# Kernel tuning notes

Hardware: AMD Instinct MI355X
Metric: run time of the kernel (lower is better)

## Reference

```python
import jax, jax.numpy as jnp
import numpy as np

NUM_KEYS = 64

def setup_inputs() -> dict:
    key = jax.random.key(0)
    k1, k2 = jax.random.split(key)
    inputs = jax.random.randint(k1, (8, 4096, 1024), 0, NUM_KEYS, dtype=jnp.int32)
    # learned per-key bias (build() creates shape (num_keys,) for key_shape=[1])
    b = jax.random.normal(k2, (NUM_KEYS,), dtype=jnp.float32)
    # keys are sorted unique scalars (0..63), stored as float like the TF cast
    keys = jnp.arange(NUM_KEYS, dtype=jnp.float32)
    return {"inputs": inputs, "b": b, "keys": keys}


def reference(inputs, b, keys):
    # Original math: out = sum_k (inputs == keys[k]) * b[k], elementwise over inputs.
    # With unique sorted keys this is a gather: find the matching key index per
    # element and pick b there; elements matching no key contribute 0.
    # This avoids the O(num_keys * numel) broadcast blow-up of the TF graph.
    xf = inputs.astype(jnp.float32)
    K = keys.shape[0]
    idx = jnp.clip(jnp.searchsorted(keys, xf), 0, K - 1)  # [8,4096,1024]
    out = jnp.where(keys[idx] == xf, b[idx], jnp.float32(0.0))
    return out
```

## Files before the change

kernel.cpp:

```cpp
#include <hip/hip_runtime.h>

#define NKEYS 64
#define UNROLL 4

typedef int   __attribute__((ext_vector_type(4))) i32x4;
typedef float __attribute__((ext_vector_type(4))) f32x4;

__global__ __launch_bounds__(256) void sel_xform_kernel(
    const i32x4* __restrict__ in,
    const float* __restrict__ b,
    const float* __restrict__ keys,
    f32x4* __restrict__ out,
    int nvec, int ntail, const int* __restrict__ in_tail, float* __restrict__ out_tail)
{
    __shared__ float t[NKEYS];
    const int tid = threadIdx.x;
    if (tid < NKEYS) t[tid] = 0.0f;
    __syncthreads();
    if (tid < NKEYS) {
        const float kv = keys[tid];
        const int iv = (int)kv;
        if ((float)iv == kv && iv >= 0 && iv < NKEYS) {
            t[iv] = b[tid];
        }
    }
    __syncthreads();

    const int B = blockDim.x;
    const int chunk = gridDim.x * B * UNROLL;

    auto lut4 = [&](i32x4 v) -> f32x4 {
        const float rx = t[v.x & 63];
        const float ry = t[v.y & 63];
        const float rz = t[v.z & 63];
        const float rw = t[v.w & 63];
        f32x4 o;
        o.x = ((unsigned)v.x < NKEYS) ? rx : 0.0f;
        o.y = ((unsigned)v.y < NKEYS) ? ry : 0.0f;
        o.z = ((unsigned)v.z < NKEYS) ? rz : 0.0f;
        o.w = ((unsigned)v.w < NKEYS) ? rw : 0.0f;
        return o;
    };

    for (int base = blockIdx.x * B * UNROLL; base < nvec; base += chunk) {
        if (base + UNROLL * B <= nvec) {
            const int i0 = base + tid;
            const i32x4 v0 = __builtin_nontemporal_load(in + i0);
            const i32x4 v1 = __builtin_nontemporal_load(in + i0 + B);
            const i32x4 v2 = __builtin_nontemporal_load(in + i0 + 2 * B);
            const i32x4 v3 = __builtin_nontemporal_load(in + i0 + 3 * B);

            out[i0]         = lut4(v0);
            out[i0 + B]     = lut4(v1);
            out[i0 + 2 * B] = lut4(v2);
            out[i0 + 3 * B] = lut4(v3);
        } else {
            for (int j = 0; j < UNROLL; ++j) {
                const int i = base + j * B + tid;
                if (i < nvec) {
                    const i32x4 v = __builtin_nontemporal_load(in + i);
                    out[i] = lut4(v);
                }
            }
        }
    }

    if (blockIdx.x == 0 && tid < ntail) {
        const int v = in_tail[tid];
        out_tail[tid] = ((unsigned)v < NKEYS) ? t[v] : 0.0f;
    }
}

extern "C" void kernel_launch(void* const* d_in, const int* in_sizes, int n_in,
                              void* d_out, int out_size, void* d_ws, size_t ws_size,
                              hipStream_t stream) {
    const int*   x    = (const int*)d_in[0];
    const float* b    = (const float*)d_in[1];
    const float* keys = (const float*)d_in[2];
    float* out = (float*)d_out;

    const int n    = in_sizes[0];
    const int nvec = n >> 2;
    const int ntail = n & 3;

    const int block = 256;
    int grid = (nvec + block * UNROLL - 1) / (block * UNROLL);
    if (grid > 2048) grid = 2048;
    if (grid < 1) grid = 1;

    sel_xform_kernel<<<grid, block, 0, stream>>>(
        (const i32x4*)x, b, keys, (f32x4*)out,
        nvec, ntail, x + (nvec << 2), out + (nvec << 2));
}
```

Baseline: 222.6 us.

## Use contiguous per-block slices with software-pipelined prefetch and nontemporal stores

Each block now owns a contiguous slice of the vectors instead of grid-striding across the whole array. Inside the slice, the loads for the next batch are issued before the current batch is looked up and stored, a double-buffered prefetch meant to keep more memory requests in flight. Output writes also switch to nontemporal stores to reduce cache pollution. The extra live registers for the prefetch buffer may lower occupancy on this purely bandwidth-bound kernel.

```diff
diff --git a/kernel.cpp b/kernel.cpp
--- a/kernel.cpp
+++ b/kernel.cpp
@@ -11,7 +11,8 @@
     const float* __restrict__ b,
     const float* __restrict__ keys,
     f32x4* __restrict__ out,
-    int nvec, int ntail, const int* __restrict__ in_tail, float* __restrict__ out_tail)
+    int nvec, int slice, int ntail,
+    const int* __restrict__ in_tail, float* __restrict__ out_tail)
 {
     __shared__ float t[NKEYS];
     const int tid = threadIdx.x;
@@ -26,8 +27,15 @@
     }
     __syncthreads();
 
+    if (blockIdx.x == 0 && tid < ntail) {
+        const int v = in_tail[tid];
+        out_tail[tid] = ((unsigned)v < NKEYS) ? t[v] : 0.0f;
+    }
+
     const int B = blockDim.x;
-    const int chunk = gridDim.x * B * UNROLL;
+    const int begin = blockIdx.x * slice;
+    if (begin >= nvec) return;
+    const int end = (begin + slice < nvec) ? (begin + slice) : nvec;
 
     auto lut4 = [&](i32x4 v) -> f32x4 {
         const float rx = t[v.x & 63];
@@ -42,32 +50,42 @@
         return o;
     };
 
-    for (int base = blockIdx.x * B * UNROLL; base < nvec; base += chunk) {
-        if (base + UNROLL * B <= nvec) {
-            const int i0 = base + tid;
-            const i32x4 v0 = __builtin_nontemporal_load(in + i0);
-            const i32x4 v1 = __builtin_nontemporal_load(in + i0 + B);
-            const i32x4 v2 = __builtin_nontemporal_load(in + i0 + 2 * B);
-            const i32x4 v3 = __builtin_nontemporal_load(in + i0 + 3 * B);
+    auto loadb = [&](int base, i32x4* dst, bool full) {
+#pragma unroll
+        for (int j = 0; j < UNROLL; ++j) {
+            const int i = base + j * B + tid;
+            if (full || i < end) dst[j] = __builtin_nontemporal_load(in + i);
+            else                 dst[j] = i32x4{0, 0, 0, 0};
+        }
+    };
+    auto storeb = [&](int base, const i32x4* v, bool full) {
+#pragma unroll
+        for (int j = 0; j < UNROLL; ++j) {
+            const int i = base + j * B + tid;
+            if (full || i < end)
+                __builtin_nontemporal_store(lut4(v[j]), out + i);
+        }
+    };
 
-            out[i0]         = lut4(v0);
-            out[i0 + B]     = lut4(v1);
-            out[i0 + 2 * B] = lut4(v2);
-            out[i0 + 3 * B] = lut4(v3);
-        } else {
-            for (int j = 0; j < UNROLL; ++j) {
-                const int i = base + j * B + tid;
-                if (i < nvec) {
-                    const i32x4 v = __builtin_nontemporal_load(in + i);
-                    out[i] = lut4(v);
-                }
-            }
+    int base = begin;
+    i32x4 cur[UNROLL];
+    bool cur_full = (base + UNROLL * B) <= end;
+    loadb(base, cur, cur_full);
+    while (true) {
+        const int nbase = base + UNROLL * B;
+        const bool have_next = nbase < end;
+        i32x4 nxt[UNROLL];
+        bool nxt_full = false;
+        if (have_next) {
+            nxt_full = (nbase + UNROLL * B) <= end;
+            loadb(nbase, nxt, nxt_full);
         }
-    }
-
-    if (blockIdx.x == 0 && tid < ntail) {
-        const int v = in_tail[tid];
-        out_tail[tid] = ((unsigned)v < NKEYS) ? t[v] : 0.0f;
+        storeb(base, cur, cur_full);
+        if (!have_next) break;
+#pragma unroll
+        for (int j = 0; j < UNROLL; ++j) cur[j] = nxt[j];
+        cur_full = nxt_full;
+        base = nbase;
     }
 }
 
@@ -84,11 +102,16 @@
     const int ntail = n & 3;
 
     const int block = 256;
-    int grid = (nvec + block * UNROLL - 1) / (block * UNROLL);
+    const int batch = block * UNROLL;
+
+    int grid = (nvec + batch - 1) / batch;
     if (grid > 2048) grid = 2048;
     if (grid < 1) grid = 1;
+    int slice = (nvec + grid - 1) / grid;
+    slice = ((slice + batch - 1) / batch) * batch;
+    grid = (nvec + slice - 1) / slice;
 
     sel_xform_kernel<<<grid, block, 0, stream>>>(
         (const i32x4*)x, b, keys, (f32x4*)out,
-        nvec, ntail, x + (nvec << 2), out + (nvec << 2));
+        nvec, slice, ntail, x + (nvec << 2), out + (nvec << 2));
 }
```

New measurement: 227.0 us. About the same (+2.0%).
